# Optimization experiments

Measured on AMD Instinct MI355X. Metric: run time of the kernel, lower is better.

## Reference

```python
import jax, jax.numpy as jnp
import numpy as np

EPS = 1e-5

def ter_quant(w):
    # BitNet b1.58 absmean ternary quantization: scale by mean(|W|), round to {-1,0,1}, rescale.
    gamma = jnp.mean(jnp.abs(w)) + EPS
    wq = jnp.clip(jnp.round(w / gamma), -1.0, 1.0) * gamma
    return wq

def setup_inputs() -> dict:
    key = jax.random.key(0)
    k_x, k_w1, k_w2 = jax.random.split(key, 3)
    B, S, D, H = 64, 197, 768, 3072
    x = jax.random.normal(k_x, (B, S, D), dtype=jnp.float32)
    w1 = jax.random.normal(k_w1, (H, D), dtype=jnp.float32) * (1.0 / np.sqrt(D))
    b1 = jnp.zeros((H,), dtype=jnp.float32)
    w2 = jax.random.normal(k_w2, (D, H), dtype=jnp.float32) * (1.0 / np.sqrt(H))
    b2 = jnp.zeros((D,), dtype=jnp.float32)
    return {"x": x, "w1": w1, "b1": b1, "w2": w2, "b2": b2}

def reference(x, w1, b1, w2, b2):
    # fc1: ternary-quantized linear, exact GELU, fc2: ternary-quantized linear (dropout p=0 is identity)
    h = jnp.einsum('bsd,hd->bsh', x, ter_quant(w1)) + b1
    h = jax.nn.gelu(h, approximate=False)
    y = jnp.einsum('bsh,dh->bsd', h, ter_quant(w2)) + b2
    return y
```

## Files before the change

### kernel.cpp

```cpp
#include <hip/hip_runtime.h>
#include <hip/hip_bf16.h>
#include <math.h>

typedef __bf16 bf16_t;
typedef __bf16 bf16x8 __attribute__((ext_vector_type(8)));
typedef __bf16 bf16x4 __attribute__((ext_vector_type(4)));
typedef float f32x4 __attribute__((ext_vector_type(4)));

#define QEPS 1e-5

__device__ __forceinline__ void gload_lds16(const void* g, void* l) {
  __builtin_amdgcn_global_load_lds((const __attribute__((address_space(1))) void*)g,
                                   (__attribute__((address_space(3))) void*)l, 16, 0, 0);
}

__device__ __forceinline__ float gelu_exact(float x) {
  float a = x * 0.7071067811865476f;
  float s = fabsf(a);
  float t = __builtin_amdgcn_rcpf(__builtin_fmaf(0.3275911f, s, 1.0f));
  float p = __builtin_fmaf(1.061405429f, t, -1.453152027f);
  p = __builtin_fmaf(p, t, 1.421413741f);
  p = __builtin_fmaf(p, t, -0.284496736f);
  p = __builtin_fmaf(p, t, 0.254829592f);
  p = p * t;
  float e = __expf(-s * s);
  float er = copysignf(__builtin_fmaf(-p, e, 1.0f), a);
  return 0.5f * x * (1.0f + er);
}

__global__ void reduce_abs2_kernel(const float* __restrict__ w1, const float* __restrict__ w2,
                                   int n, double* __restrict__ out) {
  const int nb = gridDim.x >> 1;
  const bool second = blockIdx.x >= nb;
  const float* __restrict__ w = second ? w2 : w1;
  const int b = second ? blockIdx.x - nb : blockIdx.x;
  double s = 0.0;
  const int stride = nb * blockDim.x * 4;
  for (int i = (b * blockDim.x + threadIdx.x) * 4; i < n; i += stride) {
    float4 v = *(const float4*)(w + i);
    s += (double)fabsf(v.x) + (double)fabsf(v.y) + (double)fabsf(v.z) + (double)fabsf(v.w);
  }
  for (int off = 32; off > 0; off >>= 1)
    s += __shfl_down(s, off, 64);
  __shared__ double ls[4];
  int lane = threadIdx.x & 63, wv = threadIdx.x >> 6;
  if (lane == 0) ls[wv] = s;
  __syncthreads();
  if (threadIdx.x == 0)
    atomicAdd(out + (second ? 1 : 0), ls[0] + ls[1] + ls[2] + ls[3]);
}

__global__ void quantize2_kernel(const float* __restrict__ w1, const float* __restrict__ w2,
                                 int n, const double* __restrict__ sums, double cnt,
                                 bf16_t* __restrict__ q1, bf16_t* __restrict__ q2) {
  int i4 = blockIdx.x * blockDim.x + threadIdx.x;
  const int half4 = n >> 2;
  const float* w;
  bf16_t* q;
  double g;
  int idx;
  if (i4 < half4) { w = w1; q = q1; g = sums[0]; idx = i4; }
  else            { w = w2; q = q2; g = sums[1]; idx = i4 - half4; }
  g = g / cnt + QEPS;
  float4 v = ((const float4*)w)[idx];
  bf16x4 r;
  {
    double t0 = fmin(1.0, fmax(-1.0, rint((double)v.x / g)));
    double t1 = fmin(1.0, fmax(-1.0, rint((double)v.y / g)));
    double t2 = fmin(1.0, fmax(-1.0, rint((double)v.z / g)));
    double t3 = fmin(1.0, fmax(-1.0, rint((double)v.w / g)));
    r[0] = (bf16_t)(float)t0; r[1] = (bf16_t)(float)t1;
    r[2] = (bf16_t)(float)t2; r[3] = (bf16_t)(float)t3;
  }
  ((bf16x4*)q)[idx] = r;
}

__global__ void cast_pad_kernel(const float* __restrict__ x, bf16_t* __restrict__ xb,
                                long long nvalid, long long ntotal) {
  long long i = ((long long)blockIdx.x * blockDim.x + threadIdx.x) * 4;
  if (i >= ntotal) return;
  bf16x4 r;
  if (i < nvalid) {
    float4 v = *(const float4*)(x + i);
    r[0] = (bf16_t)v.x; r[1] = (bf16_t)v.y; r[2] = (bf16_t)v.z; r[3] = (bf16_t)v.w;
  } else {
    r[0] = (bf16_t)0.0f; r[1] = (bf16_t)0.0f; r[2] = (bf16_t)0.0f; r[3] = (bf16_t)0.0f;
  }
  *(bf16x4*)(xb + i) = r;
}

template <int EPI>
__global__ __launch_bounds__(256, 2)
void gemm_bt_kernel(const bf16_t* __restrict__ A, const bf16_t* __restrict__ B,
                    const float* __restrict__ bias,
                    const double* __restrict__ sumptr, double cnt,
                    void* __restrict__ Cout, int N, int K, int Mvalid) {
  __shared__ bf16_t sA[128 * 64];
  __shared__ bf16_t sB[128 * 64];
  const int tid = threadIdx.x;
  const int lane = tid & 63;
  const int wave = tid >> 6;
  const int wr = (wave >> 1) * 64;
  const int wc = (wave & 1) * 64;
  const int row16 = lane & 15;
  const int quad = lane >> 4;

  const size_t Ks = (size_t)K;
  const int slot = tid & 7;
  const int cg = slot ^ ((tid >> 3) & 7);
  const bf16_t* gA = A + ((size_t)(blockIdx.y * 128 + (tid >> 3))) * Ks + (size_t)cg * 8;
  const bf16_t* gB = B + ((size_t)(blockIdx.x * 128 + (tid >> 3))) * Ks + (size_t)cg * 8;
  bf16_t* lA = sA + wave * 512;
  bf16_t* lB = sB + wave * 512;

  f32x4 acc[4][4] = {};

  for (int k0 = 0; k0 < K; k0 += 64) {
#pragma unroll
    for (int n = 0; n < 4; n++) {
      gload_lds16(gA + (size_t)(n * 32) * Ks, lA + n * 2048);
      gload_lds16(gB + (size_t)(n * 32) * Ks, lB + n * 2048);
    }
    gA += 64;
    gB += 64;
    __syncthreads();

#pragma unroll
    for (int kk = 0; kk < 2; kk++) {
      bf16x8 afr[4], bfr[4];
      const int swz = ((kk * 4 + quad) ^ (row16 & 7)) * 8;
#pragma unroll
      for (int i = 0; i < 4; i++)
        afr[i] = *(const bf16x8*)&sA[(wr + i * 16 + row16) * 64 + swz];
#pragma unroll
      for (int j = 0; j < 4; j++)
        bfr[j] = *(const bf16x8*)&sB[(wc + j * 16 + row16) * 64 + swz];
#pragma unroll
      for (int i = 0; i < 4; i++)
#pragma unroll
        for (int j = 0; j < 4; j++)
          acc[i][j] = __builtin_amdgcn_mfma_f32_16x16x32_bf16(afr[i], bfr[j], acc[i][j], 0, 0, 0);
    }
    __syncthreads();
  }

  const float gamma = (float)(sumptr[0] / cnt + QEPS);
  const int c_base = blockIdx.x * 128 + wc + row16;
  const int r_base = blockIdx.y * 128 + wr + quad * 4;

  if constexpr (EPI == 0) {
    __shared__ bf16_t sE[32 * 136];
    float bv[4];
#pragma unroll
    for (int j = 0; j < 4; j++) bv[j] = bias[c_base + j * 16];
    bf16_t* h = (bf16_t*)Cout;
#pragma unroll
    for (int i = 0; i < 4; i++) {
#pragma unroll
      for (int j = 0; j < 4; j++) {
        const int col = wc + j * 16 + row16;
#pragma unroll
        for (int r = 0; r < 4; r++) {
          const int e = (wave >> 1) * 16 + quad * 4 + r;
          float v = gelu_exact(gamma * acc[i][j][r] + bv[j]);
          sE[e * 136 + col] = (bf16_t)v;
        }
      }
      __syncthreads();
      {
        const int e = tid >> 3, ch = tid & 7;
        const int grow = blockIdx.y * 128 + (e >> 4) * 64 + i * 16 + (e & 15);
        bf16_t* dst = &h[(size_t)grow * N + blockIdx.x * 128];
        *(bf16x8*)&dst[ch * 8] = *(const bf16x8*)&sE[e * 136 + ch * 8];
        *(bf16x8*)&dst[ch * 8 + 64] = *(const bf16x8*)&sE[e * 136 + ch * 8 + 64];
      }
      __syncthreads();
    }
  } else {
    float* out = (float*)Cout;
#pragma unroll
    for (int j = 0; j < 4; j++) {
      const int col = c_base + j * 16;
      const float bv = bias[col];
#pragma unroll
      for (int i = 0; i < 4; i++) {
#pragma unroll
        for (int r = 0; r < 4; r++) {
          const int row = r_base + i * 16 + r;
          if (row < Mvalid)
            out[(size_t)row * N + col] = gamma * acc[i][j][r] + bv;
        }
      }
    }
  }
}

extern "C" void kernel_launch(void* const* d_in, const int* in_sizes, int n_in,
                              void* d_out, int out_size, void* d_ws, size_t ws_size,
                              hipStream_t stream) {
  const float* x  = (const float*)d_in[0];
  const float* w1 = (const float*)d_in[1];
  const float* b1 = (const float*)d_in[2];
  const float* w2 = (const float*)d_in[3];
  const float* b2 = (const float*)d_in[4];
  float* out = (float*)d_out;

  const int M = 64 * 197;
  const int Mpad = 12672;
  const int D = 768, H = 3072;
  const int nW = H * D;

  char* ws = (char*)d_ws;
  double* sums = (double*)ws;
  bf16_t* xb  = (bf16_t*)(ws + 256);
  bf16_t* w1q = xb + (size_t)Mpad * D;
  bf16_t* w2q = w1q + (size_t)H * D;
  bf16_t* hb  = w2q + (size_t)D * H;

  hipMemsetAsync(sums, 0, 2 * sizeof(double), stream);
  reduce_abs2_kernel<<<512, 256, 0, stream>>>(w1, w2, nW, sums);
  quantize2_kernel<<<(2 * nW / 4) / 256, 256, 0, stream>>>(w1, w2, nW, sums, (double)nW, w1q, w2q);
  cast_pad_kernel<<<((long long)Mpad * D / 4) / 256, 256, 0, stream>>>(
      x, xb, (long long)M * D, (long long)Mpad * D);

  dim3 g1(H / 128, Mpad / 128);
  gemm_bt_kernel<0><<<g1, 256, 0, stream>>>(xb, w1q, b1, sums + 0, (double)nW, hb, H, D, M);
  dim3 g2(D / 128, Mpad / 128);
  gemm_bt_kernel<1><<<g2, 256, 0, stream>>>(hb, w2q, b2, sums + 1, (double)nW, out, D, H, M);
}
```

Before: 288.5 us.

## Remap GEMM blocks per XCD, raise occupancy target, reuse LDS for epilogue

```diff
diff --git a/kernel.cpp b/kernel.cpp
--- a/kernel.cpp
+++ b/kernel.cpp
@@ -90,13 +90,23 @@
 }
 
 template <int EPI>
-__global__ __launch_bounds__(256, 2)
+__global__ __launch_bounds__(256, 4)
 void gemm_bt_kernel(const bf16_t* __restrict__ A, const bf16_t* __restrict__ B,
                     const float* __restrict__ bias,
                     const double* __restrict__ sumptr, double cnt,
-                    void* __restrict__ Cout, int N, int K, int Mvalid) {
+                    void* __restrict__ Cout, int N, int K, int Mvalid, int gx) {
   __shared__ bf16_t sA[128 * 64];
   __shared__ bf16_t sB[128 * 64];
+
+  const int G = gridDim.x;
+  const int f = blockIdx.x;
+  const int xcd = f & 7;
+  const int idx = f >> 3;
+  const int q8 = G >> 3, r8 = G & 7;
+  const int t = xcd * q8 + (xcd < r8 ? xcd : r8) + idx;
+  const int bx = t % gx;
+  const int by = t / gx;
+
   const int tid = threadIdx.x;
   const int lane = tid & 63;
   const int wave = tid >> 6;
@@ -108,8 +118,8 @@
   const size_t Ks = (size_t)K;
   const int slot = tid & 7;
   const int cg = slot ^ ((tid >> 3) & 7);
-  const bf16_t* gA = A + ((size_t)(blockIdx.y * 128 + (tid >> 3))) * Ks + (size_t)cg * 8;
-  const bf16_t* gB = B + ((size_t)(blockIdx.x * 128 + (tid >> 3))) * Ks + (size_t)cg * 8;
+  const bf16_t* gA = A + ((size_t)(by * 128 + (tid >> 3))) * Ks + (size_t)cg * 8;
+  const bf16_t* gB = B + ((size_t)(bx * 128 + (tid >> 3))) * Ks + (size_t)cg * 8;
   bf16_t* lA = sA + wave * 512;
   bf16_t* lB = sB + wave * 512;
 
@@ -145,11 +155,11 @@
   }
 
   const float gamma = (float)(sumptr[0] / cnt + QEPS);
-  const int c_base = blockIdx.x * 128 + wc + row16;
-  const int r_base = blockIdx.y * 128 + wr + quad * 4;
+  const int c_base = bx * 128 + wc + row16;
+  const int r_base = by * 128 + wr + quad * 4;
 
   if constexpr (EPI == 0) {
-    __shared__ bf16_t sE[32 * 136];
+    bf16_t* sE = sA;
     float bv[4];
 #pragma unroll
     for (int j = 0; j < 4; j++) bv[j] = bias[c_base + j * 16];
@@ -169,8 +179,8 @@
       __syncthreads();
       {
         const int e = tid >> 3, ch = tid & 7;
-        const int grow = blockIdx.y * 128 + (e >> 4) * 64 + i * 16 + (e & 15);
-        bf16_t* dst = &h[(size_t)grow * N + blockIdx.x * 128];
+        const int grow = by * 128 + (e >> 4) * 64 + i * 16 + (e & 15);
+        bf16_t* dst = &h[(size_t)grow * N + bx * 128];
         *(bf16x8*)&dst[ch * 8] = *(const bf16x8*)&sE[e * 136 + ch * 8];
         *(bf16x8*)&dst[ch * 8 + 64] = *(const bf16x8*)&sE[e * 136 + ch * 8 + 64];
       }
@@ -223,8 +233,9 @@
   cast_pad_kernel<<<((long long)Mpad * D / 4) / 256, 256, 0, stream>>>(
       x, xb, (long long)M * D, (long long)Mpad * D);
 
-  dim3 g1(H / 128, Mpad / 128);
-  gemm_bt_kernel<0><<<g1, 256, 0, stream>>>(xb, w1q, b1, sums + 0, (double)nW, hb, H, D, M);
-  dim3 g2(D / 128, Mpad / 128);
-  gemm_bt_kernel<1><<<g2, 256, 0, stream>>>(hb, w2q, b2, sums + 1, (double)nW, out, D, H, M);
-}
+  const int gy = Mpad / 128;
+  const int gx1 = H / 128;
+  const int gx2 = D / 128;
+  gemm_bt_kernel<0><<<gx1 * gy, 256, 0, stream>>>(xb, w1q, b1, sums + 0, (double)nW, hb, H, D, M, gx1);
+  gemm_bt_kernel<1><<<gx2 * gy, 256, 0, stream>>>(hb, w2q, b2, sums + 1, (double)nW, out, D, H, M, gx2);
+}
```

Result: faster. 262.7 us (-8.9%).
